# Performance work log

Measured on AMD Instinct MI355X. Metric: run time of the kernel, lower is better.

Reference implementation:

```python
import jax, jax.numpy as jnp
import numpy as np
import math

N_HEADS = 8
EPS = 1e-12


def _ln(x, g, b):
    m = x.mean(-1, keepdims=True)
    v = ((x - m) ** 2).mean(-1, keepdims=True)
    return (x - m) * jax.lax.rsqrt(v + EPS) * g + b


def _ffn(x, w1, b1, w2, b2):
    # torch nn.GELU default = exact erf gelu; dropout is identity in eval
    return jax.nn.gelu(x @ w1 + b1, approximate=False) @ w2 + b2


def _mha(q_in, kv, mask, qw, qb, kw, kb, vw, vb, ow, ob):
    B, S, _ = q_in.shape
    dh = qw.shape[1] // N_HEADS

    def split(x):
        return x.reshape(B, S, N_HEADS, dh).transpose(0, 2, 1, 3)  # (B,H,S,dh)

    q = split(q_in @ qw + qb) / math.sqrt(dh)
    k = split(kv @ kw + kb)
    v = split(kv @ vw + vb)
    scores = jnp.einsum('bhqd,bhkd->bhqk', q, k) + mask[:, None]
    w = jax.nn.softmax(scores, axis=-1)
    ctx = jnp.einsum('bhqk,bhkd->bhqd', w, v)
    ctx = ctx.transpose(0, 2, 1, 3).reshape(B, S, N_HEADS * dh)
    return ctx @ ow + ob


def reference(hidden, lens,
              f_ffn_w1, f_ffn_b1, f_ffn_w2, f_ffn_b2, f_ln_g, f_ln_b,
              f_q_w, f_q_b, f_k_w, f_k_b, f_v_w, f_v_b, f_o_w, f_o_b,
              b_ffn_w1, b_ffn_b1, b_ffn_w2, b_ffn_b2, b_ln_g, b_ln_b,
              b_q_w, b_q_b, b_k_w, b_k_b, b_v_w, b_v_b, b_o_w, b_o_b,
              attn_ln_g, attn_ln_b,
              out_ffn_w1, out_ffn_b1, out_ffn_w2, out_ffn_b2,
              out_ln_g, out_ln_b):
    S, B, D2 = hidden.shape
    H = D2 // 2
    S2 = S - 2
    f = hidden[..., :H]
    bk = hidden[..., H:]
    query = jnp.concatenate([f[:-2], bk[2:]], axis=-1)        # (S2, B, 2H)
    qbf = jnp.swapaxes(query, 0, 1)                            # (B, S2, 2H)

    # vectorized per-sample length-dependent masks (additive, 0 / -inf)
    qi = jnp.arange(S2)[:, None]
    ki = jnp.arange(S2)[None, :]
    Lm = (lens - 2)[:, None, None]
    # forward: rows >= L-2 all zero; valid rows causal (k <= q) inside [0, L-2)
    f_mask = jnp.where((qi >= Lm) | (ki <= qi), 0.0, -np.inf).astype(hidden.dtype)
    # backward: rows >= L-2 all zero; valid rows anti-causal (k >= q) with k < L-2
    b_mask = jnp.where((qi >= Lm) | ((ki >= qi) & (ki < Lm)), 0.0, -np.inf).astype(hidden.dtype)

    f_q = _ln(_ffn(qbf, f_ffn_w1, f_ffn_b1, f_ffn_w2, f_ffn_b2), f_ln_g, f_ln_b)
    f_kv = jnp.swapaxes(f[:-2], 0, 1)
    f_attn = _mha(f_q, f_kv, f_mask, f_q_w, f_q_b, f_k_w, f_k_b, f_v_w, f_v_b, f_o_w, f_o_b)

    b_q = _ln(_ffn(qbf, b_ffn_w1, b_ffn_b1, b_ffn_w2, b_ffn_b2), b_ln_g, b_ln_b)
    b_kv = jnp.swapaxes(bk[2:], 0, 1)
    b_attn = _mha(b_q, b_kv, b_mask, b_q_w, b_q_b, b_k_w, b_k_b, b_v_w, b_v_b, b_o_w, b_o_b)

    attn_out = _ln(qbf + jnp.concatenate([f_attn, b_attn], axis=-1), attn_ln_g, attn_ln_b)
    out = _ln(_ffn(attn_out, out_ffn_w1, out_ffn_b1, out_ffn_w2, out_ffn_b2), out_ln_g, out_ln_b)
    return jnp.swapaxes(out, 0, 1)                             # (S2, B, 2H)


def setup_inputs():
    key = jax.random.key(0)
    ks = jax.random.split(key, 16)
    S, B, H = 1024, 8, 512
    d = {}
    d['hidden'] = jax.random.normal(ks[0], (S, B, 2 * H), jnp.float32)
    d['lens'] = jax.random.randint(ks[1], (B,), 4, S + 1)

    def w(k, i, o):
        return jax.random.normal(k, (i, o), jnp.float32) * 0.02

    idx = 2
    for p in ('f', 'b'):
        d[p + '_ffn_w1'] = w(ks[idx], 2 * H, 2 * H); idx += 1
        d[p + '_ffn_b1'] = jnp.zeros((2 * H,), jnp.float32)
        d[p + '_ffn_w2'] = w(ks[idx], 2 * H, H); idx += 1
        d[p + '_ffn_b2'] = jnp.zeros((H,), jnp.float32)
        d[p + '_ln_g'] = jnp.ones((H,), jnp.float32)
        d[p + '_ln_b'] = jnp.zeros((H,), jnp.float32)
        for n in ('q', 'k', 'v', 'o'):
            d[p + '_' + n + '_w'] = w(jax.random.fold_in(ks[idx], hash(n) % 97), H, H)
            d[p + '_' + n + '_b'] = jnp.zeros((H,), jnp.float32)
        idx += 1
    d['attn_ln_g'] = jnp.ones((2 * H,), jnp.float32)
    d['attn_ln_b'] = jnp.zeros((2 * H,), jnp.float32)
    d['out_ffn_w1'] = w(ks[idx], 2 * H, 2 * H); idx += 1
    d['out_ffn_b1'] = jnp.zeros((2 * H,), jnp.float32)
    d['out_ffn_w2'] = w(ks[idx], 2 * H, 2 * H); idx += 1
    d['out_ffn_b2'] = jnp.zeros((2 * H,), jnp.float32)
    d['out_ln_g'] = jnp.ones((2 * H,), jnp.float32)
    d['out_ln_b'] = jnp.zeros((2 * H,), jnp.float32)
    return d
```

## Files before the change

### kernel.cpp

```cpp
#include <hip/hip_runtime.h>
#include <cmath>

#define S_ 1024
#define B_ 8
#define H_ 512
#define S2_ 1022
#define M_ (B_*S2_)
#define PAD_ 8192
#define VTS_ ((size_t)8*8*64*1024)

typedef __attribute__((ext_vector_type(8))) short bf16x8;
typedef __attribute__((ext_vector_type(4))) float f32x4;
typedef __attribute__((ext_vector_type(4))) unsigned int u32x4;
typedef __attribute__((ext_vector_type(2))) unsigned int u32x2;

__device__ __forceinline__ unsigned short f2bf(float f){
  unsigned int u = __float_as_uint(f);
  return (unsigned short)((u + 0x7fffu + ((u>>16)&1u)) >> 16);
}
__device__ __forceinline__ float bf2f(unsigned short u){
  return __uint_as_float((unsigned int)u << 16);
}
__device__ __forceinline__ float fgelu(float x){
  float u = x * (0.7978845608f + 0.0356774081f * x * x);
  return x / (1.f + __expf(-2.f * u));
}
__device__ __forceinline__ float fexp2(float x){
  float r; asm("v_exp_f32 %0, %1" : "=v"(r) : "v"(x)); return r;
}
__device__ __forceinline__ unsigned int cvtpk(float lo, float hi){
  unsigned int r; asm("v_cvt_pk_bf16_f32 %0, %1, %2" : "=v"(r) : "v"(lo), "v"(hi)); return r;
}

__device__ __forceinline__ void glds16(const void* g, void* l){
  __builtin_amdgcn_global_load_lds((const __attribute__((address_space(1))) unsigned int*)g,
                                   (__attribute__((address_space(3))) unsigned int*)l, 16, 0, 0);
}
#define SB() __builtin_amdgcn_sched_barrier(0)

__global__ __launch_bounds__(256) void lma_prep_x(const float* __restrict__ hidden,
                                                  unsigned short* __restrict__ Xb){
  int m = blockIdx.x; int dq = threadIdx.x * 4;
  int b = m / S2_, s = m - b * S2_;
  int srow = (dq < 512) ? s : (s + 2);
  const float* src = hidden + ((size_t)srow * B_ + b) * 1024 + dq;
  f32x4 v = *(const f32x4*)src;
  union { u32x2 u; unsigned short s4[4]; } pk;
  #pragma unroll
  for (int j = 0; j < 4; j++) pk.s4[j] = f2bf(v[j]);
  *(u32x2*)&Xb[(size_t)m * 1024 + dq] = pk.u;
}

struct TPack {
  const float* src[14];
  unsigned short* dst[14];
  int K[14];
  int N[14];
};
__global__ __launch_bounds__(256) void lma_transpose_all(TPack p){
  int idx = blockIdx.z;
  int K = p.K[idx], N = p.N[idx];
  int kb = blockIdx.x * 32, nb = blockIdx.y * 32;
  if (kb >= K || nb >= N) return;
  const float* W = p.src[idx];
  unsigned short* WT = p.dst[idx];
  __shared__ float t[32][33];
  int tx = threadIdx.x & 31, ty = threadIdx.x >> 5;
  #pragma unroll
  for (int i = ty; i < 32; i += 8) t[i][tx] = W[(size_t)(kb + i) * N + nb + tx];
  __syncthreads();
  #pragma unroll
  for (int i = ty; i < 32; i += 8) WT[(size_t)(nb + i) * K + kb + tx] = f2bf(t[tx][i]);
}

__global__ __launch_bounds__(256) void lma_biascat(const float* __restrict__ fk, const float* __restrict__ fv,
                                                   const float* __restrict__ bk, const float* __restrict__ bv,
                                                   float* __restrict__ out){
  int i = blockIdx.x * 256 + threadIdx.x;
  int fb = i >> 10, col = i & 1023;
  const float* s = (col < 512) ? (fb ? bk : fk) : (fb ? bv : fv);
  out[i] = s[col & 511];
}

__global__ __launch_bounds__(256) void lma_vt2(const unsigned short* __restrict__ KV2,
                                               unsigned short* __restrict__ VT2){
  __shared__ unsigned short t[32][34];
  int s0 = blockIdx.x * 32, c0 = blockIdx.y * 32;
  int z = blockIdx.z, fb = z >> 3, b = z & 7;
  const unsigned short* V = KV2 + (size_t)fb * PAD_ * 1024 + 512;
  unsigned short* VT = VT2 + (size_t)fb * VTS_;
  int tx = threadIdx.x & 31, ty = threadIdx.x >> 5;
  #pragma unroll
  for (int i = ty; i < 32; i += 8){
    int s = s0 + i; if (s > S2_-1) s = S2_-1;
    t[i][tx] = V[((size_t)b * S2_ + s) * 1024 + c0 + tx];
  }
  __syncthreads();
  int s = s0 + tx;
  #pragma unroll
  for (int i = ty; i < 32; i += 8){
    int c = c0 + i, h = c >> 6, d = c & 63;
    VT[(((size_t)b * 8 + h) * 64 + d) * 1024 + s] = (s < S2_) ? t[tx][i] : (unsigned short)0;
  }
}

__global__ __launch_bounds__(256) void lma_gemm2(
    const unsigned short* __restrict__ A, int lda,
    const unsigned short* __restrict__ Bt0, const unsigned short* __restrict__ Bt1,
    const float* __restrict__ bias0, const float* __restrict__ bias1,
    void* __restrict__ Cout, int ldc,
    int M, int N, int K, int mode, int amap, int nmt)
{
  __shared__ unsigned short Al[128*32];
  __shared__ unsigned short Bl[128*32];
  const int tid = threadIdx.x;
  const int w = tid >> 6, lane = tid & 63, quad = lane >> 4, l16 = lane & 15;
  const int mt = blockIdx.x % nmt, nt = blockIdx.x / nmt;
  const int m0 = mt * 128, n0 = nt * 128;
  const int brch = m0 >> 13;
  const unsigned short* Bt = brch ? Bt1 : Bt0;
  const float* bias = brch ? bias1 : bias0;
  const int coloff = (amap == 2 && brch) ? 512 : 0;
  const int wm = (w >> 1) * 64, wn = (w & 1) * 64;

  f32x4 acc[4][4];
  #pragma unroll
  for (int i = 0; i < 4; i++)
    #pragma unroll
    for (int f = 0; f < 4; f++) acc[i][f] = f32x4{0.f,0.f,0.f,0.f};

  const int srow = lane >> 2;
  const int spc  = (((lane & 3) ^ ((lane >> 2) & 3))) * 8;
  const int rswz = (l16 & 3);

  for (int k0 = 0; k0 < K; k0 += 32) {
    #pragma unroll
    for (int c = 0; c < 2; c++) {
      int ra = w*32 + c*16 + srow;
      int ga = m0 + ra;
      int ar;
      if (amap == 0) { ar = (ga > M-1) ? (M-1) : ga; }
      else { ar = ga & (PAD_-1); if (ar > M_-1) ar = M_-1; }
      glds16(A + (size_t)ar * lda + coloff + k0 + spc, &Al[(w*32 + c*16) * 32]);
      int gb = n0 + ra; if (gb > N-1) gb = N-1;
      glds16(Bt + (size_t)gb * K + k0 + spc, &Bl[(w*32 + c*16) * 32]);
    }
    __syncthreads();
    bf16x8 af[4], bfr[4];
    #pragma unroll
    for (int i = 0; i < 4; i++) af[i]  = *(const bf16x8*)&Al[(wm + i*16 + l16)*32 + ((quad ^ rswz) * 8)];
    #pragma unroll
    for (int f = 0; f < 4; f++) bfr[f] = *(const bf16x8*)&Bl[(wn + f*16 + l16)*32 + ((quad ^ rswz) * 8)];
    #pragma unroll
    for (int i = 0; i < 4; i++)
      #pragma unroll
      for (int f = 0; f < 4; f++)
        acc[i][f] = __builtin_amdgcn_mfma_f32_16x16x32_bf16(af[i], bfr[f], acc[i][f], 0, 0, 0);
    __syncthreads();
  }

  #pragma unroll
  for (int f = 0; f < 4; f++) {
    int col = n0 + wn + f*16 + l16;
    float bv = bias ? bias[col] : 0.f;
    #pragma unroll
    for (int i = 0; i < 4; i++) {
      #pragma unroll
      for (int r = 0; r < 4; r++) {
        int row = m0 + wm + i*16 + quad*4 + r;
        if (row < M) {
          float v = acc[i][f][r] + bv;
          if (mode == 2) v = fgelu(v);
          else if (mode == 1) v *= 0.18033688011112042f;
          if (mode <= 2) ((unsigned short*)Cout)[(size_t)row * ldc + col] = f2bf(v);
          else if (mode == 3) ((float*)Cout)[(size_t)row * ldc + col] = v;
          else {
            int sr = row % S2_, bb2 = row / S2_;
            ((float*)Cout)[((size_t)sr * B_ + bb2) * ldc + col] = v;
          }
        }
      }
    }
  }
}

__global__ __launch_bounds__(512, 2) void lma_gemm8(
    const unsigned short* __restrict__ A, int lda,
    const unsigned short* __restrict__ Bt0, const unsigned short* __restrict__ Bt1,
    const float* __restrict__ bias0, const float* __restrict__ bias1,
    unsigned short* __restrict__ Cout, int ldc,
    int M, int N, int K, int mode, int amap, int nmt)
{
  __shared__ unsigned short Ls[2][2][256*64];
  const int tid = threadIdx.x;
  const int w = tid >> 6, lane = tid & 63, quad = lane >> 4, l16 = lane & 15;
  const int mt = blockIdx.x % nmt, nt = blockIdx.x / nmt;
  const int m0 = mt * 256, n0 = nt * 256;
  const int brch = m0 >> 13;
  const unsigned short* Bt = brch ? Bt1 : Bt0;
  const float* bias = brch ? bias1 : bias0;
  const int coloff = (amap == 2 && brch) ? 512 : 0;
  const int wm = (w >> 2) * 128, wn = (w & 3) * 64;

  f32x4 acc[8][4];
  #pragma unroll
  for (int i = 0; i < 8; i++)
    #pragma unroll
    for (int f = 0; f < 4; f++) acc[i][f] = f32x4{0.f,0.f,0.f,0.f};

  const int lrow8 = lane >> 3;
  const int lkb   = lane & 7;
  const int NT = K >> 6;

  auto stageA = [&](int buf, int hf, int kt){
    #pragma unroll
    for (int c = 0; c < 2; c++){
      int rt = (w>>2)*128 + hf*64 + ((w&3)*2 + c)*8 + lrow8;
      int kb = lkb ^ (((rt>>2)&3)<<1);
      int ga = m0 + rt;
      int ar;
      if (amap == 0) { ar = (ga > M-1) ? (M-1) : ga; }
      else { ar = ga & (PAD_-1); if (ar > M_-1) ar = M_-1; }
      glds16(A + (size_t)ar * lda + coloff + kt*64 + kb*8,
             &Ls[buf][0][((w>>2)*128 + hf*64 + ((w&3)*2 + c)*8) * 64]);
    }
  };
  auto stageB = [&](int buf, int hf, int kt){
    #pragma unroll
    for (int c = 0; c < 2; c++){
      int rt = (w>>1)*64 + hf*32 + ((w&1)*2 + c)*8 + lrow8;
      int kb = lkb ^ (((rt>>2)&3)<<1);
      int gb = n0 + rt; if (gb > N-1) gb = N-1;
      glds16(Bt + (size_t)gb * K + kt*64 + kb*8,
             &Ls[buf][1][((w>>1)*64 + hf*32 + ((w&1)*2 + c)*8) * 64]);
    }
  };

  bf16x8 af[4][2], bf0[2][2], bf1[2][2];

  #define LDA8(buf, mq) { _Pragma("unroll") for (int j = 0; j < 4; j++){ \
      int rt = wm + (mq)*64 + j*16 + l16; \
      const unsigned short* base = &Ls[buf][0][rt*64]; \
      int f_ = ((rt>>2)&3)<<1; \
      af[j][0] = *(const bf16x8*)(base + ((    quad) ^ f_)*8); \
      af[j][1] = *(const bf16x8*)(base + ((4 + quad) ^ f_)*8); } }
  #define LDB8(buf, nq, dst) { _Pragma("unroll") for (int j = 0; j < 2; j++){ \
      int rt = wn + (nq)*32 + j*16 + l16; \
      const unsigned short* base = &Ls[buf][1][rt*64]; \
      int f_ = ((rt>>2)&3)<<1; \
      dst[j][0] = *(const bf16x8*)(base + ((    quad) ^ f_)*8); \
      dst[j][1] = *(const bf16x8*)(base + ((4 + quad) ^ f_)*8); } }
  #define MFMAQ(mq, nq, bfr) { __builtin_amdgcn_s_setprio(1); \
      _Pragma("unroll") for (int j = 0; j < 4; j++) \
        _Pragma("unroll") for (int j2 = 0; j2 < 2; j2++){ \
          acc[(mq)*4+j][(nq)*2+j2] = __builtin_amdgcn_mfma_f32_16x16x32_bf16(af[j][0], bfr[j2][0], acc[(mq)*4+j][(nq)*2+j2], 0, 0, 0); \
          acc[(mq)*4+j][(nq)*2+j2] = __builtin_amdgcn_mfma_f32_16x16x32_bf16(af[j][1], bfr[j2][1], acc[(mq)*4+j][(nq)*2+j2], 0, 0, 0); } \
      __builtin_amdgcn_s_setprio(0); }
  #define BAR()   { SB(); __builtin_amdgcn_s_barrier(); SB(); }
  #define LGKM0() { asm volatile("s_waitcnt lgkmcnt(0)" ::: "memory"); SB(); }
  #define VM4()   { asm volatile("s_waitcnt vmcnt(4)"   ::: "memory"); SB(); }

  stageA(0, 0, 0); stageB(0, 0, 0); stageA(0, 1, 0); stageB(0, 1, 0);
  stageA(1, 0, 1); stageB(1, 0, 1);
  VM4(); BAR();

  const int NI = NT >> 1;
  for (int i = 0; i < NI; i++) {
    const int tb  = 2*i + 1;
    int ta2 = 2*i + 2; if (ta2 > NT-1) ta2 = NT-1;
    int tb2 = 2*i + 3; if (tb2 > NT-1) tb2 = NT-1;

    LDA8(0, 0); LDB8(0, 0, bf0); stageA(1, 1, tb);
    BAR(); LGKM0(); MFMAQ(0, 0, bf0); BAR();
    LDB8(0, 1, bf1); stageB(1, 1, tb);
    BAR(); LGKM0(); MFMAQ(0, 1, bf1); BAR();
    LDA8(0, 1); stageA(0, 0, ta2);
    BAR(); LGKM0(); MFMAQ(1, 0, bf0); BAR();
    stageB(0, 0, ta2);
    BAR(); MFMAQ(1, 1, bf1); VM4(); BAR();
    LDA8(1, 0); LDB8(1, 0, bf0); stageA(0, 1, ta2);
    BAR(); LGKM0(); MFMAQ(0, 0, bf0); BAR();
    LDB8(1, 1, bf1); stageB(0, 1, ta2);
    BAR(); LGKM0(); MFMAQ(0, 1, bf1); BAR();
    LDA8(1, 1); stageA(1, 0, tb2);
    BAR(); LGKM0(); MFMAQ(1, 0, bf0); BAR();
    stageB(1, 0, tb2);
    BAR(); MFMAQ(1, 1, bf1); VM4(); BAR();
  }
  asm volatile("s_waitcnt vmcnt(0)" ::: "memory");

  #pragma unroll
  for (int f = 0; f < 4; f++) {
    int col = n0 + wn + f*16 + l16;
    float bv = bias ? bias[col] : 0.f;
    #pragma unroll
    for (int i2 = 0; i2 < 8; i2++) {
      #pragma unroll
      for (int r = 0; r < 4; r++) {
        int row = m0 + wm + i2*16 + quad*4 + r;
        if (row < M) {
          float v = acc[i2][f][r] + bv;
          if (mode == 2) v = fgelu(v);
          Cout[(size_t)row * ldc + col] = f2bf(v);
        }
      }
    }
  }
  #undef LDA8
  #undef LDB8
  #undef MFMAQ
  #undef BAR
  #undef LGKM0
  #undef VM4
}

__device__ __forceinline__ void lma_red2(float& s, float& sq){
  __shared__ float red[16];
  #pragma unroll
  for (int msk = 1; msk < 64; msk <<= 1){ s += __shfl_xor(s, msk); sq += __shfl_xor(sq, msk); }
  int w = threadIdx.x >> 6;
  if ((threadIdx.x & 63) == 0){ red[w] = s; red[8 + w] = sq; }
  __syncthreads();
  s  = red[0] + red[1] + red[2] + red[3];
  sq = red[8] + red[9] + red[10] + red[11];
}

__global__ __launch_bounds__(256) void lma_ln(const float* __restrict__ in,
                                              const float* __restrict__ g, const float* __restrict__ bb,
                                              int D, unsigned short* __restrict__ obf, float* __restrict__ of32){
  int row = blockIdx.x, t = threadIdx.x;
  const float* x = in + (size_t)row * D;
  float s = 0.f, sq = 0.f;
  for (int d = t; d < D; d += 256){ float v = x[d]; s += v; sq += v * v; }
  lma_red2(s, sq);
  float mean = s / D;
  float var = sq / D - mean * mean;
  float rstd = rsqrtf(fmaxf(var, 0.f) + 1e-12f);
  if (obf) {
    for (int d = t; d < D; d += 256) obf[(size_t)row * D + d] = f2bf((x[d] - mean) * rstd * g[d] + bb[d]);
  } else {
    for (int d = t; d < D; d += 256) of32[(size_t)row * D + d] = (x[d] - mean) * rstd * g[d] + bb[d];
  }
}

__global__ __launch_bounds__(256) void lma_ln2(const unsigned short* __restrict__ T12b,
                                               const float* __restrict__ fg, const float* __restrict__ fbb,
                                               const float* __restrict__ bg, const float* __restrict__ bbb,
                                               unsigned short* __restrict__ LQ2){
  int m = blockIdx.x, t = threadIdx.x;
  int fb = (m >= M_);
  int idx = m - fb * M_;
  const float* g = fb ? bg : fg;
  const float* bb = fb ? bbb : fbb;
  const unsigned short* x = T12b + ((size_t)fb * PAD_ + idx) * 512;
  unsigned short* o = LQ2 + ((size_t)fb * PAD_ + idx) * 512;
  float v0 = bf2f(x[t]), v1 = bf2f(x[t + 256]);
  float s = v0 + v1, sq = v0*v0 + v1*v1;
  lma_red2(s, sq);
  float mean = s / 512.f;
  float var = sq / 512.f - mean * mean;
  float rstd = rsqrtf(fmaxf(var, 0.f) + 1e-12f);
  o[t]       = f2bf((v0 - mean) * rstd * g[t]       + bb[t]);
  o[t + 256] = f2bf((v1 - mean) * rstd * g[t + 256] + bb[t + 256]);
}

__global__ __launch_bounds__(256) void lma_attn_ln(const unsigned short* __restrict__ pf,
                                                   const unsigned short* __restrict__ pb,
                                                   const float* __restrict__ hidden,
                                                   const float* __restrict__ g, const float* __restrict__ bb,
                                                   unsigned short* __restrict__ out){
  int m = blockIdx.x, t = threadIdx.x;
  int b = m / S2_, s = m - b * S2_;
  const float* hf = hidden + ((size_t)s       * B_ + b) * 1024;
  const float* hb = hidden + ((size_t)(s + 2) * B_ + b) * 1024;
  float v[4]; float sum = 0.f, sq = 0.f;
  #pragma unroll
  for (int j = 0; j < 4; j++){
    int d = t + j * 256;
    float x = (d < 512) ? (bf2f(pf[(size_t)m * 512 + d]) + hf[d])
                        : (bf2f(pb[(size_t)m * 512 + (d - 512)]) + hb[d]);
    v[j] = x; sum += x; sq += x * x;
  }
  lma_red2(sum, sq);
  float mean = sum / 1024.f;
  float var = sq / 1024.f - mean * mean;
  float rstd = rsqrtf(fmaxf(var, 0.f) + 1e-12f);
  #pragma unroll
  for (int j = 0; j < 4; j++){
    int d = t + j * 256;
    out[(size_t)m * 1024 + d] = f2bf((v[j] - mean) * rstd * g[d] + bb[d]);
  }
}

__global__ __launch_bounds__(256, 4) void lma_attn9(const unsigned short* __restrict__ Q2,
                                                    const unsigned short* __restrict__ KV2,
                                                    const unsigned short* __restrict__ VT2,
                                                    unsigned short* __restrict__ CT2,
                                                    const int* __restrict__ lens,
                                                    int fb){
  __shared__ unsigned short Kl[64*64];
  __shared__ unsigned short Vl[64*64];
  __shared__ __align__(16) unsigned short Pl[4][16*64];

  const int tid = threadIdx.x;
  const int w = tid >> 6, lane = tid & 63, quad = lane >> 4, l16 = lane & 15;
  const int id = blockIdx.x;
  const int qt = id >> 6, h = (id >> 3) & 7, b = id & 7;
  const int backward = fb;
  const int L2 = lens[b] - 2;
  const int q0wg = qt * 64;
  const int q0 = q0wg + w * 16;
  const int qg = q0 + l16;
  const int qload = (qg > S2_-1) ? (S2_-1) : qg;

  const size_t qbase  = ((size_t)b * S2_) * 512  + h * 64;
  const size_t kbase  = ((size_t)b * S2_) * 1024 + h * 64;
  const size_t vtbase = ((size_t)(b * 8 + h) * 64) * 1024;
  char* Pb = (char*)&Pl[w][0];

  const int lrow = lane >> 3;
  const int g0s  = (lane & 7) ^ lrow;
  const int x7   = l16 & 7;
  const int x7s  = x7 << 4;

  const unsigned short* Q  = Q2  + (size_t)fb * PAD_ * 512;
  const unsigned short* Kx = KV2 + (size_t)fb * PAD_ * 1024;
  const unsigned short* VT = VT2 + (size_t)fb * VTS_;
  unsigned short* CTX      = CT2 + (size_t)fb * PAD_ * 512;

  bf16x8 qf[2];
  {
    const unsigned short* qp = Q + qbase + (size_t)qload * 512 + quad * 8;
    qf[0] = *(const bf16x8*)(qp);
    qf[1] = *(const bf16x8*)(qp + 32);
  }

  float mi = -3e38f, li = 0.f;
  f32x4 ot[4];
  #pragma unroll
  for (int f = 0; f < 4; f++) ot[f] = f32x4{0.f,0.f,0.f,0.f};

  int klo = 0, khi = S2_ - 1;
  if (q0wg + 63 < L2) {
    if (!backward) khi = q0wg + 63;
    else { klo = q0wg; khi = L2 - 1; }
  }

  for (int kt0 = klo; kt0 <= khi; kt0 += 64) {
    #pragma unroll
    for (int c = 0; c < 2; c++) {
      int r = w*16 + c*8 + lrow;
      int kr = kt0 + r; if (kr > S2_-1) kr = S2_-1;
      glds16(Kx + kbase + (size_t)kr * 1024 + g0s * 8, &Kl[(w*16 + c*8) * 64]);
      glds16(VT + vtbase + (size_t)r * 1024 + kt0 + g0s * 8, &Vl[(w*16 + c*8) * 64]);
    }
    __syncthreads();

    bf16x8 kf[4][2], vf[4][2];
    #pragma unroll
    for (int sub = 0; sub < 4; sub++) {
      const unsigned short* kp = &Kl[(sub*16 + l16) * 64];
      kf[sub][0] = *(const bf16x8*)(kp + (( quad      ^ x7) * 8));
      kf[sub][1] = *(const bf16x8*)(kp + (((quad + 4) ^ x7) * 8));
    }
    #pragma unroll
    for (int f = 0; f < 4; f++) {
      const unsigned short* vp = &Vl[(f*16 + l16) * 64];
      vf[f][0] = *(const bf16x8*)(vp + (( quad      ^ x7) * 8));
      vf[f][1] = *(const bf16x8*)(vp + (((quad + 4) ^ x7) * 8));
    }

    f32x4 st[4];
    __builtin_amdgcn_s_setprio(1);
    #pragma unroll
    for (int sub = 0; sub < 4; sub++) {
      f32x4 s = f32x4{0.f,0.f,0.f,0.f};
      s = __builtin_amdgcn_mfma_f32_16x16x32_bf16(kf[sub][0], qf[0], s, 0, 0, 0);
      s = __builtin_amdgcn_mfma_f32_16x16x32_bf16(kf[sub][1], qf[1], s, 0, 0, 0);
      st[sub] = s;
    }
    __builtin_amdgcn_s_setprio(0);

    {
      bool tail = (kt0 + 63 > S2_ - 1);
      bool full;
      if (!backward) full = !tail && ((kt0 + 63 <= q0) || (q0 >= L2));
      else           full = !tail && ((q0 >= L2) || ((kt0 >= q0 + 15) && (kt0 + 63 < L2)));
      if (!full) {
        #pragma unroll
        for (int sub = 0; sub < 4; sub++) {
          #pragma unroll
          for (int r = 0; r < 4; r++) {
            int kg = kt0 + sub*16 + quad*4 + r;
            bool ok;
            if (!backward) ok = (kg < S2_) && ((qg >= L2) || (kg <= qg));
            else           ok = (kg < S2_) && ((qg >= L2) || ((kg >= qg) && (kg < L2)));
            if (!ok) st[sub][r] = -3e38f;
          }
        }
      }
    }

    float mx = -3e38f;
    #pragma unroll
    for (int sub = 0; sub < 4; sub++)
      #pragma unroll
      for (int r = 0; r < 4; r++) mx = fmaxf(mx, st[sub][r]);
    mx = fmaxf(mx, __shfl_xor(mx, 16));
    mx = fmaxf(mx, __shfl_xor(mx, 32));

    if (__any(mx > mi + 11.f)) {
      float mn = fmaxf(mi, mx);
      float al = fexp2(mi - mn);
      li *= al;
      #pragma unroll
      for (int f = 0; f < 4; f++)
        #pragma unroll
        for (int r = 0; r < 4; r++) ot[f][r] *= al;
      mi = mn;
    }

    float rs = 0.f;
    #pragma unroll
    for (int sub = 0; sub < 4; sub++)
      #pragma unroll
      for (int r = 0; r < 4; r++) {
        float p = fexp2(st[sub][r] - mi);
        st[sub][r] = p; rs += p;
      }
    rs += __shfl_xor(rs, 16);
    rs += __shfl_xor(rs, 32);
    li += rs;

    #pragma unroll
    for (int sub = 0; sub < 4; sub++) {
      u32x2 pk2;
      pk2[0] = cvtpk(st[sub][0], st[sub][1]);
      pk2[1] = cvtpk(st[sub][2], st[sub][3]);
      *(u32x2*)(Pb + (l16*128 + ((sub*32 + quad*8) ^ x7s))) = pk2;
    }
    bf16x8 pfr0 = *(const bf16x8*)(Pb + (l16*128 + (( 0 + quad*16) ^ x7s)));
    bf16x8 pfr1 = *(const bf16x8*)(Pb + (l16*128 + ((64 + quad*16) ^ x7s)));

    __builtin_amdgcn_s_setprio(1);
    #pragma unroll
    for (int f = 0; f < 4; f++) {
      ot[f] = __builtin_amdgcn_mfma_f32_16x16x32_bf16(vf[f][0], pfr0, ot[f], 0, 0, 0);
      ot[f] = __builtin_amdgcn_mfma_f32_16x16x32_bf16(vf[f][1], pfr1, ot[f], 0, 0, 0);
    }
    __builtin_amdgcn_s_setprio(0);
    __syncthreads();
  }

  if (qg < S2_) {
    float rcp = 1.f / li;
    #pragma unroll
    for (int f = 0; f < 4; f++) {
      ushort4 pk;
      pk.x = f2bf(ot[f][0] * rcp); pk.y = f2bf(ot[f][1] * rcp);
      pk.z = f2bf(ot[f][2] * rcp); pk.w = f2bf(ot[f][3] * rcp);
      *(ushort4*)&CTX[qbase + (size_t)qg * 512 + f*16 + quad*4] = pk;
    }
  }
}

extern "C" void kernel_launch(void* const* d_in, const int* in_sizes, int n_in,
                              void* d_out, int out_size, void* d_ws, size_t ws_size,
                              hipStream_t stream)
{
  const float* hidden = (const float*)d_in[0];
  const int*   lens   = (const int*)d_in[1];
  const float* fw[14]; for (int i = 0; i < 14; i++) fw[i] = (const float*)d_in[2 + i];
  const float* bw[14]; for (int i = 0; i < 14; i++) bw[i] = (const float*)d_in[16 + i];
  const float* attn_g = (const float*)d_in[30];
  const float* attn_b = (const float*)d_in[31];
  const float* o_w1 = (const float*)d_in[32];
  const float* o_b1 = (const float*)d_in[33];
  const float* o_w2 = (const float*)d_in[34];
  const float* o_b2 = (const float*)d_in[35];
  const float* o_lng = (const float*)d_in[36];
  const float* o_lnb = (const float*)d_in[37];

  char* ws = (char*)d_ws;
  size_t off = 0;
  auto alloc = [&](size_t bytes)->char* {
    off = (off + 255) & ~(size_t)255;
    char* p = ws + off; off += bytes; return p;
  };

  unsigned short* fw1t = (unsigned short*)alloc((size_t)1024*1024*2);
  unsigned short* fw2t = (unsigned short*)alloc((size_t)512*1024*2);
  unsigned short* fqt  = (unsigned short*)alloc((size_t)512*512*2);
  unsigned short* fkvt = (unsigned short*)alloc((size_t)1024*512*2);
  unsigned short* fot  = (unsigned short*)alloc((size_t)512*512*2);
  unsigned short* bw1t = (unsigned short*)alloc((size_t)1024*1024*2);
  unsigned short* bw2t = (unsigned short*)alloc((size_t)512*1024*2);
  unsigned short* bqt  = (unsigned short*)alloc((size_t)512*512*2);
  unsigned short* bkvt = (unsigned short*)alloc((size_t)1024*512*2);
  unsigned short* bot  = (unsigned short*)alloc((size_t)512*512*2);
  unsigned short* ow1t = (unsigned short*)alloc((size_t)1024*1024*2);
  unsigned short* ow2t = (unsigned short*)alloc((size_t)1024*1024*2);
  float*          biasKV = (float*)alloc(2048*4);

  unsigned short* Xb   = (unsigned short*)alloc((size_t)M_*1024*2);
  unsigned short* big1 = (unsigned short*)alloc((size_t)2*PAD_*1024*2);
  float*          big2 = (float*)alloc((size_t)2*PAD_*512*4);
  unsigned short* LQCT = (unsigned short*)alloc((size_t)2*PAD_*512*2);
  unsigned short* Q2   = (unsigned short*)alloc((size_t)2*PAD_*512*2);

  unsigned short* H12 = big1, *KV2 = big1, *H1o = big1;
  unsigned short* T12b = (unsigned short*)big2;
  unsigned short* VT2  = (unsigned short*)big2;
  unsigned short* P2b  = (unsigned short*)big2 + 2*VTS_;
  unsigned short* LQ2 = LQCT, *CT2 = LQCT;

  lma_prep_x<<<M_, 256, 0, stream>>>(hidden, Xb);

  {
    TPack tp;
    const float* srcs[14] = { fw[0], fw[2], fw[6], fw[8], fw[10], fw[12],
                              bw[0], bw[2], bw[6], bw[8], bw[10], bw[12],
                              o_w1, o_w2 };
    unsigned short* dsts[14] = { fw1t, fw2t, fqt, fkvt, fkvt + (size_t)512*512, fot,
                                 bw1t, bw2t, bqt, bkvt, bkvt + (size_t)512*512, bot,
                                 ow1t, ow2t };
    int Ks[14] = {1024,1024,512,512,512,512, 1024,1024,512,512,512,512, 1024,1024};
    int Ns[14] = {1024, 512,512,512,512,512, 1024, 512,512,512,512,512, 1024,1024};
    for (int i = 0; i < 14; i++){ tp.src[i]=srcs[i]; tp.dst[i]=dsts[i]; tp.K[i]=Ks[i]; tp.N[i]=Ns[i]; }
    lma_transpose_all<<<dim3(32, 32, 14), 256, 0, stream>>>(tp);
  }
  lma_biascat<<<8, 256, 0, stream>>>(fw[9], fw[11], bw[9], bw[11], biasKV);

  auto G = [&](const unsigned short* A, int lda,
               const unsigned short* B0, const unsigned short* B1,
               const float* b0, const float* b1,
               void* C, int ldc, int M, int N, int K, int mode, int amap){
    int nmt = (M + 127) / 128;
    lma_gemm2<<<dim3(nmt * (N/128)), 256, 0, stream>>>(A, lda, B0, B1, b0, b1, C, ldc, M, N, K, mode, amap, nmt);
  };
  auto G8 = [&](const unsigned short* A, int lda,
                const unsigned short* B0, const unsigned short* B1,
                const float* b0, const float* b1,
                unsigned short* C, int ldc, int M, int N, int K, int mode, int amap){
    int nmt = M / 256;
    lma_gemm8<<<dim3(nmt * (N/256)), 512, 0, stream>>>(A, lda, B0, B1, b0, b1, C, ldc, M, N, K, mode, amap, nmt);
  };

  G8(Xb, 1024, fw1t, bw1t, fw[1], bw[1], H12, 1024, 2*PAD_, 1024, 1024, 2, 1);
  G(H12, 1024, fw2t, bw2t, fw[3], bw[3], T12b, 512, 2*PAD_, 512, 1024, 0, 0);
  lma_ln2<<<2*M_, 256, 0, stream>>>(T12b, fw[4], fw[5], bw[4], bw[5], LQ2);
  G(LQ2, 512, fqt, bqt, fw[7], bw[7], Q2, 512, 2*PAD_, 512, 512, 1, 0);
  G8(Xb, 1024, fkvt, bkvt, biasKV, biasKV + 1024, KV2, 1024, 2*PAD_, 1024, 512, 0, 2);
  lma_vt2<<<dim3(32, 16, 16), 256, 0, stream>>>(KV2, VT2);

  lma_attn9<<<dim3(1024), 256, 0, stream>>>(Q2, KV2, VT2, CT2, lens, 0);
  lma_attn9<<<dim3(1024), 256, 0, stream>>>(Q2, KV2, VT2, CT2, lens, 1);

  G(CT2, 512, fot, bot, fw[13], bw[13], P2b, 512, 2*PAD_, 512, 512, 0, 0);

  lma_attn_ln<<<M_, 256, 0, stream>>>(P2b, P2b + (size_t)PAD_*512, hidden, attn_g, attn_b, Xb);

  G(Xb, 1024, ow1t, ow1t, o_b1, o_b1, H1o, 1024, M_, 1024, 1024, 2, 0);
  G(H1o, 1024, ow2t, ow2t, o_b2, o_b2, (float*)d_out, 1024, M_, 1024, 1024, 4, 0);
  lma_ln<<<M_, 256, 0, stream>>>((float*)d_out, o_lng, o_lnb, 1024, nullptr, (float*)d_out);
}
```

Baseline: 627.8 us.

## Reorder GEMM stage/MFMA schedule with precomputed load pointers and permute attention tile order

The GEMM main loop now precomputes the global and LDS addresses for the async loads once, outside the loop. It drops the second B-fragment register set and reorders the quadrant MFMAs in a snake pattern so B fragments are reloaded instead of held in extra registers. The global-to-LDS staging is respread across the sub-steps with new vmcnt wait thresholds (6 and 2), which changes the prefetch depth. Separately, attention blocks map their query tile index through a fixed permutation to balance causal-mask work across the grid. This lowers register pressure and address arithmetic but adds extra LDS reads for B and risks pipeline hazards if the wait counts are wrong.

```diff
diff --git a/kernel.cpp b/kernel.cpp
--- a/kernel.cpp
+++ b/kernel.cpp
@@ -212,57 +212,60 @@
   const int lkb   = lane & 7;
   const int NT = K >> 6;
 
-  auto stageA = [&](int buf, int hf, int kt){
-    #pragma unroll
-    for (int c = 0; c < 2; c++){
-      int rt = (w>>2)*128 + hf*64 + ((w&3)*2 + c)*8 + lrow8;
-      int kb = lkb ^ (((rt>>2)&3)<<1);
-      int ga = m0 + rt;
+  const unsigned short* aP[2][2]; const unsigned short* bP[2][2];
+  int aD[2][2], bD[2][2];
+  #pragma unroll
+  for (int hf = 0; hf < 2; hf++)
+    #pragma unroll
+    for (int c = 0; c < 2; c++) {
+      int rtA = (w>>2)*128 + hf*64 + ((w&3)*2 + c)*8 + lrow8;
+      int kbA = lkb ^ (((rtA>>2)&3)<<1);
+      int ga = m0 + rtA;
       int ar;
       if (amap == 0) { ar = (ga > M-1) ? (M-1) : ga; }
       else { ar = ga & (PAD_-1); if (ar > M_-1) ar = M_-1; }
-      glds16(A + (size_t)ar * lda + coloff + kt*64 + kb*8,
-             &Ls[buf][0][((w>>2)*128 + hf*64 + ((w&3)*2 + c)*8) * 64]);
-    }
-  };
-  auto stageB = [&](int buf, int hf, int kt){
-    #pragma unroll
-    for (int c = 0; c < 2; c++){
-      int rt = (w>>1)*64 + hf*32 + ((w&1)*2 + c)*8 + lrow8;
-      int kb = lkb ^ (((rt>>2)&3)<<1);
-      int gb = n0 + rt; if (gb > N-1) gb = N-1;
-      glds16(Bt + (size_t)gb * K + kt*64 + kb*8,
-             &Ls[buf][1][((w>>1)*64 + hf*32 + ((w&1)*2 + c)*8) * 64]);
-    }
-  };
-
-  bf16x8 af[4][2], bf0[2][2], bf1[2][2];
-
+      aP[hf][c] = A + (size_t)ar * lda + coloff + kbA*8;
+      aD[hf][c] = ((w>>2)*128 + hf*64 + ((w&3)*2 + c)*8) * 64;
+      int rtB = (w>>1)*64 + hf*32 + ((w&1)*2 + c)*8 + lrow8;
+      int kbB = lkb ^ (((rtB>>2)&3)<<1);
+      int gb = n0 + rtB; if (gb > N-1) gb = N-1;
+      bP[hf][c] = Bt + (size_t)gb * K + kbB*8;
+      bD[hf][c] = ((w>>1)*64 + hf*32 + ((w&1)*2 + c)*8) * 64;
+    }
+
+  bf16x8 af[4][2], bf[2][2];
+
+  #define STA(buf, hf, kt) { _Pragma("unroll") for (int c = 0; c < 2; c++) \
+      glds16(aP[hf][c] + (size_t)(kt)*64, &Ls[buf][0][aD[hf][c]]); }
+  #define STB(buf, hf, kt) { _Pragma("unroll") for (int c = 0; c < 2; c++) \
+      glds16(bP[hf][c] + (size_t)(kt)*64, &Ls[buf][1][bD[hf][c]]); }
   #define LDA8(buf, mq) { _Pragma("unroll") for (int j = 0; j < 4; j++){ \
       int rt = wm + (mq)*64 + j*16 + l16; \
       const unsigned short* base = &Ls[buf][0][rt*64]; \
       int f_ = ((rt>>2)&3)<<1; \
       af[j][0] = *(const bf16x8*)(base + ((    quad) ^ f_)*8); \
       af[j][1] = *(const bf16x8*)(base + ((4 + quad) ^ f_)*8); } }
-  #define LDB8(buf, nq, dst) { _Pragma("unroll") for (int j = 0; j < 2; j++){ \
+  #define LDB8(buf, nq) { _Pragma("unroll") for (int j = 0; j < 2; j++){ \
       int rt = wn + (nq)*32 + j*16 + l16; \
       const unsigned short* base = &Ls[buf][1][rt*64]; \
       int f_ = ((rt>>2)&3)<<1; \
-      dst[j][0] = *(const bf16x8*)(base + ((    quad) ^ f_)*8); \
-      dst[j][1] = *(const bf16x8*)(base + ((4 + quad) ^ f_)*8); } }
-  #define MFMAQ(mq, nq, bfr) { __builtin_amdgcn_s_setprio(1); \
+      bf[j][0] = *(const bf16x8*)(base + ((    quad) ^ f_)*8); \
+      bf[j][1] = *(const bf16x8*)(base + ((4 + quad) ^ f_)*8); } }
+  #define MFMAQ(mq, nq) { __builtin_amdgcn_s_setprio(1); \
       _Pragma("unroll") for (int j = 0; j < 4; j++) \
         _Pragma("unroll") for (int j2 = 0; j2 < 2; j2++){ \
-          acc[(mq)*4+j][(nq)*2+j2] = __builtin_amdgcn_mfma_f32_16x16x32_bf16(af[j][0], bfr[j2][0], acc[(mq)*4+j][(nq)*2+j2], 0, 0, 0); \
-          acc[(mq)*4+j][(nq)*2+j2] = __builtin_amdgcn_mfma_f32_16x16x32_bf16(af[j][1], bfr[j2][1], acc[(mq)*4+j][(nq)*2+j2], 0, 0, 0); } \
+          acc[(mq)*4+j][(nq)*2+j2] = __builtin_amdgcn_mfma_f32_16x16x32_bf16(af[j][0], bf[j2][0], acc[(mq)*4+j][(nq)*2+j2], 0, 0, 0); \
+          acc[(mq)*4+j][(nq)*2+j2] = __builtin_amdgcn_mfma_f32_16x16x32_bf16(af[j][1], bf[j2][1], acc[(mq)*4+j][(nq)*2+j2], 0, 0, 0); } \
       __builtin_amdgcn_s_setprio(0); }
   #define BAR()   { SB(); __builtin_amdgcn_s_barrier(); SB(); }
   #define LGKM0() { asm volatile("s_waitcnt lgkmcnt(0)" ::: "memory"); SB(); }
-  #define VM4()   { asm volatile("s_waitcnt vmcnt(4)"   ::: "memory"); SB(); }
-
-  stageA(0, 0, 0); stageB(0, 0, 0); stageA(0, 1, 0); stageB(0, 1, 0);
-  stageA(1, 0, 1); stageB(1, 0, 1);
-  VM4(); BAR();
+  #define VM6()   { asm volatile("s_waitcnt vmcnt(6)"   ::: "memory"); SB(); }
+  #define VM2()   { asm volatile("s_waitcnt vmcnt(2)"   ::: "memory"); SB(); }
+
+  STA(0, 0, 0); STB(0, 0, 0); STB(0, 1, 0); STA(0, 1, 0);
+  STA(1, 0, 1);
+  asm volatile("s_waitcnt vmcnt(2)" ::: "memory"); SB();
+  BAR();
 
   const int NI = NT >> 1;
   for (int i = 0; i < NI; i++) {
@@ -270,22 +273,22 @@
     int ta2 = 2*i + 2; if (ta2 > NT-1) ta2 = NT-1;
     int tb2 = 2*i + 3; if (tb2 > NT-1) tb2 = NT-1;
 
-    LDA8(0, 0); LDB8(0, 0, bf0); stageA(1, 1, tb);
-    BAR(); LGKM0(); MFMAQ(0, 0, bf0); BAR();
-    LDB8(0, 1, bf1); stageB(1, 1, tb);
-    BAR(); LGKM0(); MFMAQ(0, 1, bf1); BAR();
-    LDA8(0, 1); stageA(0, 0, ta2);
-    BAR(); LGKM0(); MFMAQ(1, 0, bf0); BAR();
-    stageB(0, 0, ta2);
-    BAR(); MFMAQ(1, 1, bf1); VM4(); BAR();
-    LDA8(1, 0); LDB8(1, 0, bf0); stageA(0, 1, ta2);
-    BAR(); LGKM0(); MFMAQ(0, 0, bf0); BAR();
-    LDB8(1, 1, bf1); stageB(0, 1, ta2);
-    BAR(); LGKM0(); MFMAQ(0, 1, bf1); BAR();
-    LDA8(1, 1); stageA(1, 0, tb2);
-    BAR(); LGKM0(); MFMAQ(1, 0, bf0); BAR();
-    stageB(1, 0, tb2);
-    BAR(); MFMAQ(1, 1, bf1); VM4(); BAR();
+    LDA8(0, 0); LDB8(0, 0); STB(1, 0, tb); STB(1, 1, tb); STA(1, 1, tb);
+    BAR(); LGKM0(); MFMAQ(0, 0); BAR();
+    LDB8(0, 1); STA(0, 0, ta2);
+    BAR(); LGKM0(); MFMAQ(0, 1); BAR();
+    LDA8(0, 1); STB(0, 1, ta2);
+    BAR(); LGKM0(); MFMAQ(1, 1); BAR();
+    LDB8(0, 0); STA(0, 1, ta2);
+    BAR(); LGKM0(); MFMAQ(1, 0); VM6(); BAR();
+    LDA8(1, 0); LDB8(1, 0); STB(0, 0, ta2);
+    BAR(); LGKM0(); MFMAQ(0, 0); BAR();
+    LDB8(1, 1); STA(1, 0, tb2);
+    BAR(); LGKM0(); MFMAQ(0, 1); BAR();
+    LDA8(1, 1);
+    BAR(); LGKM0(); MFMAQ(1, 1); BAR();
+    LDB8(1, 0);
+    BAR(); LGKM0(); MFMAQ(1, 0); VM2(); BAR();
   }
   asm volatile("s_waitcnt vmcnt(0)" ::: "memory");
 
@@ -306,12 +309,15 @@
       }
     }
   }
+  #undef STA
+  #undef STB
   #undef LDA8
   #undef LDB8
   #undef MFMAQ
   #undef BAR
   #undef LGKM0
-  #undef VM4
+  #undef VM6
+  #undef VM2
 }
 
 __device__ __forceinline__ void lma_red2(float& s, float& sq){
@@ -405,7 +411,9 @@
   const int tid = threadIdx.x;
   const int w = tid >> 6, lane = tid & 63, quad = lane >> 4, l16 = lane & 15;
   const int id = blockIdx.x;
-  const int qt = id >> 6, h = (id >> 3) & 7, b = id & 7;
+  const int qi = id >> 6;
+  const int qt = (int)((0x8ACE75319BDF6420ull >> (qi*4)) & 15ull);
+  const int h = (id >> 3) & 7, b = id & 7;
   const int backward = fb;
   const int L2 = lens[b] - 2;
   const int q0wg = qt * 64;
```

Result: no change. 638.0 us (+1.6%).
